# Kernel optimization log

Measured on AMD Instinct MI355X. Metric: run time of the kernel, lower is better.

## Reference

```python
import jax, jax.numpy as jnp
import numpy as np
import math

D_MODEL = 1024
N_HEADS = 16
D_K = 64
D_V = 64
B = 4
S = 1024


def setup_inputs() -> dict:
    key = jax.random.key(0)
    ks = jax.random.split(key, 11)
    # xavier-ish init scale for projections
    s_in = 1.0 / math.sqrt(D_MODEL)
    return {
        "queries": jax.random.normal(ks[0], (B, S, D_MODEL), jnp.float32),
        "keys": jax.random.normal(ks[1], (B, S, D_MODEL), jnp.float32),
        "values": jax.random.normal(ks[2], (B, S, D_MODEL), jnp.float32),
        "Wq": jax.random.normal(ks[3], (D_MODEL, N_HEADS * D_K), jnp.float32) * s_in,
        "bq": jnp.zeros((N_HEADS * D_K,), jnp.float32),
        "Wk": jax.random.normal(ks[4], (D_MODEL, N_HEADS * D_K), jnp.float32) * s_in,
        "bk": jnp.zeros((N_HEADS * D_K,), jnp.float32),
        "Wv": jax.random.normal(ks[5], (D_MODEL, N_HEADS * D_V), jnp.float32) * s_in,
        "bv": jnp.zeros((N_HEADS * D_V,), jnp.float32),
        "Wo": jax.random.normal(ks[6], (N_HEADS * D_V, D_MODEL), jnp.float32) * (1.0 / math.sqrt(N_HEADS * D_V)),
        "bo": jnp.zeros((D_MODEL,), jnp.float32),
    }


def reference(queries, keys, values, Wq, bq, Wk, bk, Wv, bv, Wo, bo):
    Bq, Sq, _ = queries.shape
    Sk = keys.shape[1]
    scale = 1.0 / math.sqrt(D_K)
    # projections -> [B, S, H, d]
    q = (queries @ Wq + bq).reshape(Bq, Sq, N_HEADS, D_K)
    k = (keys @ Wk + bk).reshape(Bq, Sk, N_HEADS, D_K)
    v = (values @ Wv + bv).reshape(Bq, Sk, N_HEADS, D_V)
    # scaled dot-product attention: scores [B, H, Sq, Sk]
    scores = jnp.einsum("bqhd,bkhd->bhqk", q, k) * scale
    attn = jax.nn.softmax(scores, axis=-1)
    # weighted values -> [B, Sq, H*D_V]
    out = jnp.einsum("bhqk,bkhd->bqhd", attn, v).reshape(Bq, Sq, N_HEADS * D_V)
    return out @ Wo + bo
```

## Files before the change

kernel.cpp:

```cpp
#include <hip/hip_runtime.h>
#include <hip/hip_bf16.h>

typedef __attribute__((ext_vector_type(4))) float f32x4;
typedef __attribute__((ext_vector_type(16))) float f32x16;
typedef __attribute__((ext_vector_type(8))) short bf16x8;
typedef __attribute__((ext_vector_type(4))) unsigned short u16x4;
typedef __attribute__((ext_vector_type(8))) unsigned short u16x8;
typedef __attribute__((ext_vector_type(2))) unsigned int u32x2;

#define MFMA16(a, b, c) __builtin_amdgcn_mfma_f32_16x16x32_bf16((a), (b), (c), 0, 0, 0)
#define MFMA32(a, b, c) __builtin_amdgcn_mfma_f32_32x32x16_bf16((a), (b), (c), 0, 0, 0)

static __device__ __forceinline__ unsigned short f2bf(float f) {
    union { float f; unsigned int u; } v; v.f = f;
    unsigned int r = v.u + 0x7FFFu + ((v.u >> 16) & 1u);
    return (unsigned short)(r >> 16);
}
static __device__ __forceinline__ unsigned int pk2(float x, float y) {
    return (unsigned int)f2bf(x) | ((unsigned int)f2bf(y) << 16);
}

static __device__ __forceinline__ void gload_lds16(const void* g, void* l) {
    __builtin_amdgcn_global_load_lds(
        (const __attribute__((address_space(1))) void*)g,
        (__attribute__((address_space(3))) void*)l, 16, 0, 0);
}

__global__ __launch_bounds__(256) void convert_act(
    const float* __restrict__ q, const float* __restrict__ k,
    const float* __restrict__ v, unsigned short* __restrict__ qc,
    unsigned short* __restrict__ kc, unsigned short* __restrict__ vc) {
    const float* src = blockIdx.y == 0 ? q : (blockIdx.y == 1 ? k : v);
    unsigned short* dst = blockIdx.y == 0 ? qc : (blockIdx.y == 1 ? kc : vc);
    size_t off = ((size_t)blockIdx.x * 256 + threadIdx.x) * 8;
    f32x4 a = *(const f32x4*)&src[off];
    f32x4 b = *(const f32x4*)&src[off + 4];
    u16x8 o;
    o[0] = f2bf(a[0]); o[1] = f2bf(a[1]); o[2] = f2bf(a[2]); o[3] = f2bf(a[3]);
    o[4] = f2bf(b[0]); o[5] = f2bf(b[1]); o[6] = f2bf(b[2]); o[7] = f2bf(b[3]);
    *(u16x8*)&dst[off] = o;
}

__global__ __launch_bounds__(256) void transpose_w(
    const float* __restrict__ Wq, const float* __restrict__ Wk,
    const float* __restrict__ Wv, const float* __restrict__ Wo,
    unsigned short* __restrict__ Wt_all, unsigned short* __restrict__ Wot) {
    __shared__ unsigned short T[64][65];
    const int z = blockIdx.z;
    const float* W = z == 0 ? Wq : (z == 1 ? Wk : (z == 2 ? Wv : Wo));
    unsigned short* Wt = z < 3 ? (Wt_all + (size_t)z * 1024 * 1024) : Wot;
    const int k0 = blockIdx.y * 64, n0 = blockIdx.x * 64;
    const int t = threadIdx.x;
    const int rl = t >> 4, c4 = (t & 15) * 4;
#pragma unroll
    for (int i = 0; i < 4; ++i) {
        f32x4 v = *(const f32x4*)&W[(size_t)(k0 + rl + 16 * i) * 1024 + n0 + c4];
#pragma unroll
        for (int j = 0; j < 4; ++j) T[rl + 16 * i][c4 + j] = f2bf(v[j]);
    }
    __syncthreads();
#pragma unroll
    for (int i = 0; i < 4; ++i) {
        u16x4 o;
#pragma unroll
        for (int j = 0; j < 4; ++j) o[j] = T[c4 + j][rl + 16 * i];
        *(u16x4*)&Wt[(size_t)(n0 + rl + 16 * i) * 1024 + k0 + c4] = o;
    }
}

template <bool OUT_BF16>
__global__ __launch_bounds__(256, 2) void gemm_fast(
    const unsigned short* __restrict__ A0, const unsigned short* __restrict__ A1,
    const unsigned short* __restrict__ A2, const unsigned short* __restrict__ Wt,
    const float* __restrict__ b0, const float* __restrict__ b1,
    const float* __restrict__ b2, void* __restrict__ Outv, int ldo) {
    __shared__ __align__(16) unsigned short As[128 * 32];
    __shared__ __align__(16) unsigned short Bs[128 * 32];

    const int t = threadIdx.x;
    const int w = t >> 6, lane = t & 63;
    const int wr = w >> 1, wc = w & 1;
    const int g = lane >> 4, r15 = lane & 15;
    const int bm = blockIdx.y * 128;
    const int bn = blockIdx.x * 128;
    const int msel = bn >> 10;
    const unsigned short* A = msel == 0 ? A0 : (msel == 1 ? A1 : A2);
    const float* bias = msel == 0 ? b0 : (msel == 1 ? b1 : b2);
    const int l4 = lane >> 2, c8 = (lane & 3) * 8;

    f32x4 acc[4][4];
#pragma unroll
    for (int m = 0; m < 4; ++m)
#pragma unroll
        for (int n = 0; n < 4; ++n) acc[m][n] = (f32x4){0.f, 0.f, 0.f, 0.f};

    for (int kt = 0; kt < 1024; kt += 32) {
        __syncthreads();
        gload_lds16(&A[(size_t)(bm + 16 * w + l4) * 1024 + kt + c8], &As[w * 512]);
        gload_lds16(&A[(size_t)(bm + 16 * (w + 4) + l4) * 1024 + kt + c8], &As[(w + 4) * 512]);
        gload_lds16(&Wt[(size_t)(bn + 16 * w + l4) * 1024 + kt + c8], &Bs[w * 512]);
        gload_lds16(&Wt[(size_t)(bn + 16 * (w + 4) + l4) * 1024 + kt + c8], &Bs[(w + 4) * 512]);
        __syncthreads();
        bf16x8 af[4], bfr[4];
#pragma unroll
        for (int m = 0; m < 4; ++m)
            af[m] = *(const bf16x8*)&As[(wr * 64 + m * 16 + r15) * 32 + g * 8];
#pragma unroll
        for (int n = 0; n < 4; ++n)
            bfr[n] = *(const bf16x8*)&Bs[(wc * 64 + n * 16 + r15) * 32 + g * 8];
#pragma unroll
        for (int m = 0; m < 4; ++m)
#pragma unroll
            for (int n = 0; n < 4; ++n)
                acc[m][n] = MFMA16(af[m], bfr[n], acc[m][n]);
    }

    float* Of = (float*)Outv;
    unsigned short* Ob = (unsigned short*)Outv;
#pragma unroll
    for (int n = 0; n < 4; ++n) {
        int col = bn + wc * 64 + n * 16 + r15;
        float bv = bias[col & 1023];
#pragma unroll
        for (int m = 0; m < 4; ++m) {
#pragma unroll
            for (int r = 0; r < 4; ++r) {
                int row = bm + wr * 64 + m * 16 + g * 4 + r;
                float val = acc[m][n][r] + bv;
                if (OUT_BF16)
                    Ob[(size_t)row * ldo + col] = f2bf(val);
                else
                    Of[(size_t)row * ldo + col] = val;
            }
        }
    }
}

template <bool A_BF16, bool OUT_BF16>
__global__ __launch_bounds__(256, 2) void gemm_kernel(
    const void* __restrict__ Av, const float* __restrict__ W,
    const float* __restrict__ bias, void* __restrict__ Outv) {
    __shared__ __align__(16) unsigned short As[128][40];
    __shared__ __align__(16) unsigned short Bs[128][40];

    const int t = threadIdx.x;
    const int bm = blockIdx.y * 128;
    const int bn = blockIdx.x * 128;
    const int w = t >> 6, lane = t & 63;
    const int wr = w >> 1, wc = w & 1;
    const int g = lane >> 4, r15 = lane & 15;

    f32x4 acc[4][4];
#pragma unroll
    for (int m = 0; m < 4; ++m)
#pragma unroll
        for (int n = 0; n < 4; ++n) acc[m][n] = (f32x4){0.f, 0.f, 0.f, 0.f};

    const float* Af = (const float*)Av;
    const unsigned short* Ab = (const unsigned short*)Av;

    for (int kt = 0; kt < 1024; kt += 32) {
        __syncthreads();
#pragma unroll
        for (int i = 0; i < 4; ++i) {
            int row = (t >> 3) + i * 32;
            int c4 = (t & 7) * 4;
            if (A_BF16) {
                u16x4 v = *(const u16x4*)&Ab[(size_t)(bm + row) * 1024 + kt + c4];
                *(u16x4*)&As[row][c4] = v;
            } else {
                f32x4 v = *(const f32x4*)&Af[(size_t)(bm + row) * 1024 + kt + c4];
                u16x4 o;
                o[0] = f2bf(v[0]); o[1] = f2bf(v[1]);
                o[2] = f2bf(v[2]); o[3] = f2bf(v[3]);
                *(u16x4*)&As[row][c4] = o;
            }
        }
#pragma unroll
        for (int i = 0; i < 4; ++i) {
            int k = (t >> 5) + i * 8;
            int c4 = (t & 31) * 4;
            f32x4 v = *(const f32x4*)&W[(size_t)(kt + k) * 1024 + bn + c4];
#pragma unroll
            for (int j = 0; j < 4; ++j) Bs[c4 + j][k] = f2bf(v[j]);
        }
        __syncthreads();
        bf16x8 af[4], bfr[4];
#pragma unroll
        for (int m = 0; m < 4; ++m)
            af[m] = *(const bf16x8*)&As[wr * 64 + m * 16 + r15][g * 8];
#pragma unroll
        for (int n = 0; n < 4; ++n)
            bfr[n] = *(const bf16x8*)&Bs[wc * 64 + n * 16 + r15][g * 8];
#pragma unroll
        for (int m = 0; m < 4; ++m)
#pragma unroll
            for (int n = 0; n < 4; ++n)
                acc[m][n] = MFMA16(af[m], bfr[n], acc[m][n]);
    }

    float* Of = (float*)Outv;
    unsigned short* Ob = (unsigned short*)Outv;
#pragma unroll
    for (int n = 0; n < 4; ++n) {
        int col = bn + wc * 64 + n * 16 + r15;
        float bv = bias[col];
#pragma unroll
        for (int m = 0; m < 4; ++m) {
#pragma unroll
            for (int r = 0; r < 4; ++r) {
                int row = bm + wr * 64 + m * 16 + g * 4 + r;
                float val = acc[m][n][r] + bv;
                if (OUT_BF16)
                    Ob[(size_t)row * 1024 + col] = f2bf(val);
                else
                    Of[(size_t)row * 1024 + col] = val;
            }
        }
    }
}

__global__ __launch_bounds__(256, 2) void attn32_kernel(
    const unsigned short* __restrict__ Q, const unsigned short* __restrict__ K,
    const unsigned short* __restrict__ V, unsigned short* __restrict__ O, int ld) {
    __shared__ __align__(16) unsigned short Kls[2][64 * 80];
    __shared__ __align__(16) unsigned short Vls[2][64 * 80];

    const int t = threadIdx.x;
    const int w = t >> 6, lane = t & 63;
    const int q5 = lane & 31, hi = lane >> 5;

    const int id = blockIdx.x;
    const int sid = (id & 7) * 64 + (id >> 3);
    const int bh = sid >> 3, qb = sid & 7;
    const int b = bh >> 4, h = bh & 15;
    const int brow = b * 1024;
    const int q0 = qb * 128;

    const float c2 = 0.18033688f;

    const unsigned short* Qrow = Q + (size_t)(brow + q0 + w * 32 + q5) * ld + h * 64;
    bf16x8 qreg[8];
#pragma unroll
    for (int j = 0; j < 8; ++j) qreg[j] = *(const bf16x8*)&Qrow[8 * j];
    bf16x8 qsel[4];
#pragma unroll
    for (int kk = 0; kk < 4; ++kk) qsel[kk] = hi ? qreg[2 * kk + 1] : qreg[2 * kk];

    const int krow = t >> 2, kpart = t & 3;
    const int vkey = t & 63, vdc = t >> 6;
    const unsigned short* Kg = K + h * 64;
    const unsigned short* Vg = V + h * 64;

    u16x8 kr0, kr1, vr0, vr1;
#define STG_LOAD(KT)                                                            \
    {                                                                           \
        size_t kro = (size_t)(brow + (KT) + krow) * ld;                         \
        kr0 = *(const u16x8*)&Kg[kro + kpart * 8];                              \
        kr1 = *(const u16x8*)&Kg[kro + kpart * 8 + 32];                         \
        size_t vro = (size_t)(brow + (KT) + vkey) * ld;                         \
        vr0 = *(const u16x8*)&Vg[vro + vdc * 16];                               \
        vr1 = *(const u16x8*)&Vg[vro + vdc * 16 + 8];                           \
    }
#define STG_WRITE(BUF)                                                          \
    {                                                                           \
        char* kb_ = (char*)Kls[BUF];                                            \
        int tg_ = (krow & 7) << 4;                                              \
        *(u16x8*)(kb_ + krow * 160 + ((kpart * 16) ^ tg_)) = kr0;               \
        *(u16x8*)(kb_ + krow * 160 + (((kpart + 4) * 16) ^ tg_)) = kr1;         \
        char* vb_ = (char*)Vls[BUF];                                            \
        _Pragma("unroll") for (int j_ = 0; j_ < 8; ++j_) {                      \
            int d_ = vdc * 16 + j_;                                             \
            *(unsigned short*)(vb_ + d_ * 160 + ((vkey * 2) ^ ((d_ & 7) << 4))) \
                = vr0[j_];                                                      \
        }                                                                       \
        _Pragma("unroll") for (int j_ = 0; j_ < 8; ++j_) {                      \
            int d_ = vdc * 16 + 8 + j_;                                         \
            *(unsigned short*)(vb_ + d_ * 160 + ((vkey * 2) ^ ((d_ & 7) << 4))) \
                = vr1[j_];                                                      \
        }                                                                       \
    }

    f32x16 acc0 = {}, acc1 = {};
    float mrun = -1e30f, lrun = 0.f;

    STG_LOAD(0);
    STG_WRITE(0);
    __syncthreads();

    int cur = 0;
    for (int tile = 0; tile < 16; ++tile) {
        const bool more = tile < 15;
        if (more) STG_LOAD(tile * 64 + 64);

        char* kb = (char*)Kls[cur];
        f32x16 st0 = {}, st1 = {};
        {
            const int tg0 = (q5 & 7) << 4;
            char* kp0 = kb + q5 * 160;
            char* kp1 = kb + (q5 + 32) * 160;
#pragma unroll
            for (int kk = 0; kk < 4; ++kk) {
                int so = ((2 * kk + hi) * 16) ^ tg0;
                bf16x8 kf0 = *(const bf16x8*)(kp0 + so);
                bf16x8 kf1 = *(const bf16x8*)(kp1 + so);
                st0 = MFMA32(kf0, qsel[kk], st0);
                st1 = MFMA32(kf1, qsel[kk], st1);
            }
        }

        float mloc = st0[0];
#pragma unroll
        for (int r = 1; r < 16; ++r) mloc = fmaxf(mloc, st0[r]);
#pragma unroll
        for (int r = 0; r < 16; ++r) mloc = fmaxf(mloc, st1[r]);
        mloc = fmaxf(mloc, __shfl_xor(mloc, 32));
        float mnew = fmaxf(mrun, mloc);
        float sf = exp2f((mrun - mnew) * c2);
        mrun = mnew;
        float mneg = -mrun * c2;
        float rs = 0.f;
#pragma unroll
        for (int r = 0; r < 16; ++r) {
            st0[r] = exp2f(fmaf(st0[r], c2, mneg));
            rs += st0[r];
        }
#pragma unroll
        for (int r = 0; r < 16; ++r) {
            st1[r] = exp2f(fmaf(st1[r], c2, mneg));
            rs += st1[r];
        }
        rs += __shfl_xor(rs, 32);
        lrun = lrun * sf + rs;
#pragma unroll
        for (int r = 0; r < 16; ++r) { acc0[r] *= sf; acc1[r] *= sf; }

        char* vb = (char*)Vls[cur];
        const int tgv = (q5 & 7) << 4;
        char* vp0 = vb + q5 * 160;
        char* vp1 = vb + (q5 + 32) * 160;
#define PV_HALF(ST, CT)                                                         \
    _Pragma("unroll") for (int ks = 0; ks < 2; ++ks) {                          \
        unsigned int a0 = pk2(ST[8 * ks + 0], ST[8 * ks + 1]);                  \
        unsigned int a1 = pk2(ST[8 * ks + 2], ST[8 * ks + 3]);                  \
        unsigned int a2 = pk2(ST[8 * ks + 4], ST[8 * ks + 5]);                  \
        unsigned int a3 = pk2(ST[8 * ks + 6], ST[8 * ks + 7]);                  \
        unsigned int x0 = __shfl_xor(a0, 32), x1 = __shfl_xor(a1, 32);          \
        unsigned int x2 = __shfl_xor(a2, 32), x3 = __shfl_xor(a3, 32);          \
        union { unsigned int u[4]; bf16x8 v; } pfu;                             \
        pfu.u[0] = hi ? x2 : a0;                                                \
        pfu.u[1] = hi ? x3 : a1;                                                \
        pfu.u[2] = hi ? a2 : x0;                                                \
        pfu.u[3] = hi ? a3 : x1;                                                \
        int co = ((32 * (2 * (CT) + ks) + 16 * hi)) ^ tgv;                      \
        bf16x8 vf0 = *(const bf16x8*)(vp0 + co);                                \
        bf16x8 vf1 = *(const bf16x8*)(vp1 + co);                                \
        acc0 = MFMA32(vf0, pfu.v, acc0);                                        \
        acc1 = MFMA32(vf1, pfu.v, acc1);                                        \
    }
        PV_HALF(st0, 0);
        PV_HALF(st1, 1);

        if (more) STG_WRITE(cur ^ 1);
        __syncthreads();
        cur ^= 1;
    }

    const float inv = 1.0f / lrun;
    unsigned short* Orow = O + (size_t)(brow + q0 + w * 32 + q5) * 1024 + h * 64;
#pragma unroll
    for (int k = 0; k < 4; ++k) {
        int d0 = 8 * k + 4 * hi;
        u32x2 pa, pb;
        pa[0] = pk2(acc0[4 * k + 0] * inv, acc0[4 * k + 1] * inv);
        pa[1] = pk2(acc0[4 * k + 2] * inv, acc0[4 * k + 3] * inv);
        *(u32x2*)&Orow[d0] = pa;
        pb[0] = pk2(acc1[4 * k + 0] * inv, acc1[4 * k + 1] * inv);
        pb[1] = pk2(acc1[4 * k + 2] * inv, acc1[4 * k + 3] * inv);
        *(u32x2*)&Orow[32 + d0] = pb;
    }
#undef STG_LOAD
#undef STG_WRITE
#undef PV_HALF
}

extern "C" void kernel_launch(void* const* d_in, const int* in_sizes, int n_in,
                              void* d_out, int out_size, void* d_ws, size_t ws_size,
                              hipStream_t stream) {
    const float* q  = (const float*)d_in[0];
    const float* k  = (const float*)d_in[1];
    const float* v  = (const float*)d_in[2];
    const float* Wq = (const float*)d_in[3];
    const float* bq = (const float*)d_in[4];
    const float* Wk = (const float*)d_in[5];
    const float* bk = (const float*)d_in[6];
    const float* Wv = (const float*)d_in[7];
    const float* bv = (const float*)d_in[8];
    const float* Wo = (const float*)d_in[9];
    const float* bo = (const float*)d_in[10];

    const size_t M1 = (size_t)1024 * 1024;
    const size_t NEED = 28 * M1 * sizeof(unsigned short);

    dim3 bt(256, 1, 1);
    if (ws_size >= NEED) {
        unsigned short* qc  = (unsigned short*)d_ws;
        unsigned short* kc  = qc + 4 * M1;
        unsigned short* vc  = kc + 4 * M1;
        unsigned short* Wt  = vc + 4 * M1;
        unsigned short* Wot = Wt + 3 * M1;
        unsigned short* QKV = Wot + M1;
        unsigned short* Ob  = qc;

        convert_act<<<dim3(2048, 3), bt, 0, stream>>>(q, k, v, qc, kc, vc);
        transpose_w<<<dim3(16, 16, 4), bt, 0, stream>>>(Wq, Wk, Wv, Wo, Wt, Wot);
        gemm_fast<true><<<dim3(24, 32), bt, 0, stream>>>(qc, kc, vc, Wt, bq, bk, bv, QKV, 3072);
        attn32_kernel<<<dim3(512), bt, 0, stream>>>(QKV, QKV + 1024, QKV + 2048, Ob, 3072);
        gemm_fast<false><<<dim3(8, 32), bt, 0, stream>>>(Ob, Ob, Ob, Wot, bo, bo, bo, d_out, 1024);
    } else {
        const size_t NE = (size_t)4096 * 1024;
        unsigned short* Qb = (unsigned short*)d_ws;
        unsigned short* Kb = Qb + NE;
        unsigned short* Vb = Kb + NE;
        unsigned short* Ob = Vb + NE;
        dim3 gg(8, 32);
        gemm_kernel<false, true><<<gg, bt, 0, stream>>>(q, Wq, bq, Qb);
        gemm_kernel<false, true><<<gg, bt, 0, stream>>>(k, Wk, bk, Kb);
        gemm_kernel<false, true><<<gg, bt, 0, stream>>>(v, Wv, bv, Vb);
        attn32_kernel<<<dim3(512), bt, 0, stream>>>(Qb, Kb, Vb, Ob, 1024);
        gemm_kernel<true, false><<<gg, bt, 0, stream>>>(Ob, Wo, bo, d_out);
    }
}
```

Baseline: 229.6 us.

## Use hardware bf16 pack, lazy softmax rescale, setprio, paired V staging, narrower output GEMM tile

Replaces the software bf16 rounding with the v_cvt_pk_bf16_f32 instruction in the conversion and attention paths. In attention, the V staging now loads two adjacent keys per thread and writes packed 32-bit LDS stores. The online-softmax rescale is skipped unless the running max rises by more than a threshold, and MFMA sections are wrapped in s_setprio. The output projection GEMM uses a 64-wide N tile, giving 512 blocks instead of 256 for better CU coverage at the cost of less B-operand reuse per block.

```diff
diff --git a/kernel.cpp b/kernel.cpp
--- a/kernel.cpp
+++ b/kernel.cpp
@@ -17,7 +17,9 @@
     return (unsigned short)(r >> 16);
 }
 static __device__ __forceinline__ unsigned int pk2(float x, float y) {
-    return (unsigned int)f2bf(x) | ((unsigned int)f2bf(y) << 16);
+    unsigned int r;
+    asm("v_cvt_pk_bf16_f32 %0, %1, %2" : "=v"(r) : "v"(x), "v"(y));
+    return r;
 }
 
 static __device__ __forceinline__ void gload_lds16(const void* g, void* l) {
@@ -35,10 +37,10 @@
     size_t off = ((size_t)blockIdx.x * 256 + threadIdx.x) * 8;
     f32x4 a = *(const f32x4*)&src[off];
     f32x4 b = *(const f32x4*)&src[off + 4];
-    u16x8 o;
-    o[0] = f2bf(a[0]); o[1] = f2bf(a[1]); o[2] = f2bf(a[2]); o[3] = f2bf(a[3]);
-    o[4] = f2bf(b[0]); o[5] = f2bf(b[1]); o[6] = f2bf(b[2]); o[7] = f2bf(b[3]);
-    *(u16x8*)&dst[off] = o;
+    union { unsigned int u[4]; u16x8 v; } o;
+    o.u[0] = pk2(a[0], a[1]); o.u[1] = pk2(a[2], a[3]);
+    o.u[2] = pk2(b[0], b[1]); o.u[3] = pk2(b[2], b[3]);
+    *(u16x8*)&dst[off] = o.v;
 }
 
 __global__ __launch_bounds__(256) void transpose_w(
@@ -68,58 +70,64 @@
     }
 }
 
-template <bool OUT_BF16>
+template <bool OUT_BF16, int BN>
 __global__ __launch_bounds__(256, 2) void gemm_fast(
     const unsigned short* __restrict__ A0, const unsigned short* __restrict__ A1,
     const unsigned short* __restrict__ A2, const unsigned short* __restrict__ Wt,
     const float* __restrict__ b0, const float* __restrict__ b1,
     const float* __restrict__ b2, void* __restrict__ Outv, int ldo) {
+    constexpr int NF = BN / 32;
     __shared__ __align__(16) unsigned short As[128 * 32];
-    __shared__ __align__(16) unsigned short Bs[128 * 32];
+    __shared__ __align__(16) unsigned short Bs[BN * 32];
 
     const int t = threadIdx.x;
     const int w = t >> 6, lane = t & 63;
     const int wr = w >> 1, wc = w & 1;
     const int g = lane >> 4, r15 = lane & 15;
     const int bm = blockIdx.y * 128;
-    const int bn = blockIdx.x * 128;
+    const int bn = blockIdx.x * BN;
     const int msel = bn >> 10;
     const unsigned short* A = msel == 0 ? A0 : (msel == 1 ? A1 : A2);
     const float* bias = msel == 0 ? b0 : (msel == 1 ? b1 : b2);
     const int l4 = lane >> 2, c8 = (lane & 3) * 8;
 
-    f32x4 acc[4][4];
+    f32x4 acc[4][NF];
 #pragma unroll
     for (int m = 0; m < 4; ++m)
 #pragma unroll
-        for (int n = 0; n < 4; ++n) acc[m][n] = (f32x4){0.f, 0.f, 0.f, 0.f};
+        for (int n = 0; n < NF; ++n) acc[m][n] = (f32x4){0.f, 0.f, 0.f, 0.f};
 
     for (int kt = 0; kt < 1024; kt += 32) {
         __syncthreads();
         gload_lds16(&A[(size_t)(bm + 16 * w + l4) * 1024 + kt + c8], &As[w * 512]);
         gload_lds16(&A[(size_t)(bm + 16 * (w + 4) + l4) * 1024 + kt + c8], &As[(w + 4) * 512]);
-        gload_lds16(&Wt[(size_t)(bn + 16 * w + l4) * 1024 + kt + c8], &Bs[w * 512]);
-        gload_lds16(&Wt[(size_t)(bn + 16 * (w + 4) + l4) * 1024 + kt + c8], &Bs[(w + 4) * 512]);
+        if (BN == 128) {
+            gload_lds16(&Wt[(size_t)(bn + 16 * w + l4) * 1024 + kt + c8], &Bs[w * 512]);
+            gload_lds16(&Wt[(size_t)(bn + 16 * (w + 4) + l4) * 1024 + kt + c8],
+                        &Bs[(w + 4) * 512 % (BN * 32)]);
+        } else {
+            gload_lds16(&Wt[(size_t)(bn + 16 * w + l4) * 1024 + kt + c8], &Bs[w * 512]);
+        }
         __syncthreads();
-        bf16x8 af[4], bfr[4];
+        bf16x8 af[4], bfr[NF];
 #pragma unroll
         for (int m = 0; m < 4; ++m)
             af[m] = *(const bf16x8*)&As[(wr * 64 + m * 16 + r15) * 32 + g * 8];
 #pragma unroll
-        for (int n = 0; n < 4; ++n)
-            bfr[n] = *(const bf16x8*)&Bs[(wc * 64 + n * 16 + r15) * 32 + g * 8];
+        for (int n = 0; n < NF; ++n)
+            bfr[n] = *(const bf16x8*)&Bs[(wc * (BN / 2) + n * 16 + r15) * 32 + g * 8];
 #pragma unroll
         for (int m = 0; m < 4; ++m)
 #pragma unroll
-            for (int n = 0; n < 4; ++n)
+            for (int n = 0; n < NF; ++n)
                 acc[m][n] = MFMA16(af[m], bfr[n], acc[m][n]);
     }
 
     float* Of = (float*)Outv;
     unsigned short* Ob = (unsigned short*)Outv;
 #pragma unroll
-    for (int n = 0; n < 4; ++n) {
-        int col = bn + wc * 64 + n * 16 + r15;
+    for (int n = 0; n < NF; ++n) {
+        int col = bn + wc * (BN / 2) + n * 16 + r15;
         float bv = bias[col & 1023];
 #pragma unroll
         for (int m = 0; m < 4; ++m) {
@@ -248,7 +256,7 @@
     for (int kk = 0; kk < 4; ++kk) qsel[kk] = hi ? qreg[2 * kk + 1] : qreg[2 * kk];
 
     const int krow = t >> 2, kpart = t & 3;
-    const int vkey = t & 63, vdc = t >> 6;
+    const int vp = t & 31, vdc = t >> 5;
     const unsigned short* Kg = K + h * 64;
     const unsigned short* Vg = V + h * 64;
 
@@ -258,9 +266,9 @@
         size_t kro = (size_t)(brow + (KT) + krow) * ld;                         \
         kr0 = *(const u16x8*)&Kg[kro + kpart * 8];                              \
         kr1 = *(const u16x8*)&Kg[kro + kpart * 8 + 32];                         \
-        size_t vro = (size_t)(brow + (KT) + vkey) * ld;                         \
-        vr0 = *(const u16x8*)&Vg[vro + vdc * 16];                               \
-        vr1 = *(const u16x8*)&Vg[vro + vdc * 16 + 8];                           \
+        size_t vro = (size_t)(brow + (KT) + 2 * vp) * ld;                       \
+        vr0 = *(const u16x8*)&Vg[vro + vdc * 8];                                \
+        vr1 = *(const u16x8*)&Vg[vro + ld + vdc * 8];                           \
     }
 #define STG_WRITE(BUF)                                                          \
     {                                                                           \
@@ -270,14 +278,11 @@
         *(u16x8*)(kb_ + krow * 160 + (((kpart + 4) * 16) ^ tg_)) = kr1;         \
         char* vb_ = (char*)Vls[BUF];                                            \
         _Pragma("unroll") for (int j_ = 0; j_ < 8; ++j_) {                      \
-            int d_ = vdc * 16 + j_;                                             \
-            *(unsigned short*)(vb_ + d_ * 160 + ((vkey * 2) ^ ((d_ & 7) << 4))) \
-                = vr0[j_];                                                      \
-        }                                                                       \
-        _Pragma("unroll") for (int j_ = 0; j_ < 8; ++j_) {                      \
-            int d_ = vdc * 16 + 8 + j_;                                         \
-            *(unsigned short*)(vb_ + d_ * 160 + ((vkey * 2) ^ ((d_ & 7) << 4))) \
-                = vr1[j_];                                                      \
+            int d_ = vdc * 8 + j_;                                              \
+            unsigned int pk_ = (unsigned int)(unsigned short)vr0[j_] |          \
+                               ((unsigned int)(unsigned short)vr1[j_] << 16);   \
+            *(unsigned int*)(vb_ + d_ * 160 + ((vp * 4) ^ ((d_ & 7) << 4)))     \
+                = pk_;                                                          \
         }                                                                       \
     }
 
@@ -299,6 +304,7 @@
             const int tg0 = (q5 & 7) << 4;
             char* kp0 = kb + q5 * 160;
             char* kp1 = kb + (q5 + 32) * 160;
+            __builtin_amdgcn_s_setprio(1);
 #pragma unroll
             for (int kk = 0; kk < 4; ++kk) {
                 int so = ((2 * kk + hi) * 16) ^ tg0;
@@ -307,17 +313,23 @@
                 st0 = MFMA32(kf0, qsel[kk], st0);
                 st1 = MFMA32(kf1, qsel[kk], st1);
             }
-        }
-
-        float mloc = st0[0];
-#pragma unroll
-        for (int r = 1; r < 16; ++r) mloc = fmaxf(mloc, st0[r]);
+            __builtin_amdgcn_s_setprio(0);
+        }
+
+        float mloc = fmaxf(st0[0], st0[1]);
+#pragma unroll
+        for (int r = 2; r < 16; ++r) mloc = fmaxf(mloc, st0[r]);
 #pragma unroll
         for (int r = 0; r < 16; ++r) mloc = fmaxf(mloc, st1[r]);
         mloc = fmaxf(mloc, __shfl_xor(mloc, 32));
-        float mnew = fmaxf(mrun, mloc);
-        float sf = exp2f((mrun - mnew) * c2);
-        mrun = mnew;
+        if (!__all(mloc - mrun <= 64.f)) {
+            float mnew = fmaxf(mrun, mloc);
+            float sf = exp2f((mrun - mnew) * c2);
+            mrun = mnew;
+            lrun *= sf;
+#pragma unroll
+            for (int r = 0; r < 16; ++r) { acc0[r] *= sf; acc1[r] *= sf; }
+        }
         float mneg = -mrun * c2;
         float rs = 0.f;
 #pragma unroll
@@ -331,14 +343,13 @@
             rs += st1[r];
         }
         rs += __shfl_xor(rs, 32);
-        lrun = lrun * sf + rs;
-#pragma unroll
-        for (int r = 0; r < 16; ++r) { acc0[r] *= sf; acc1[r] *= sf; }
+        lrun += rs;
 
         char* vb = (char*)Vls[cur];
         const int tgv = (q5 & 7) << 4;
         char* vp0 = vb + q5 * 160;
         char* vp1 = vb + (q5 + 32) * 160;
+        __builtin_amdgcn_s_setprio(1);
 #define PV_HALF(ST, CT)                                                         \
     _Pragma("unroll") for (int ks = 0; ks < 2; ++ks) {                          \
         unsigned int a0 = pk2(ST[8 * ks + 0], ST[8 * ks + 1]);                  \
@@ -360,6 +371,7 @@
     }
         PV_HALF(st0, 0);
         PV_HALF(st1, 1);
+        __builtin_amdgcn_s_setprio(0);
 
         if (more) STG_WRITE(cur ^ 1);
         __syncthreads();
@@ -414,9 +426,9 @@
 
         convert_act<<<dim3(2048, 3), bt, 0, stream>>>(q, k, v, qc, kc, vc);
         transpose_w<<<dim3(16, 16, 4), bt, 0, stream>>>(Wq, Wk, Wv, Wo, Wt, Wot);
-        gemm_fast<true><<<dim3(24, 32), bt, 0, stream>>>(qc, kc, vc, Wt, bq, bk, bv, QKV, 3072);
+        gemm_fast<true, 128><<<dim3(24, 32), bt, 0, stream>>>(qc, kc, vc, Wt, bq, bk, bv, QKV, 3072);
         attn32_kernel<<<dim3(512), bt, 0, stream>>>(QKV, QKV + 1024, QKV + 2048, Ob, 3072);
-        gemm_fast<false><<<dim3(8, 32), bt, 0, stream>>>(Ob, Ob, Ob, Wot, bo, bo, bo, d_out, 1024);
+        gemm_fast<false, 64><<<dim3(16, 32), bt, 0, stream>>>(Ob, Ob, Ob, Wot, bo, bo, bo, d_out, 1024);
     } else {
         const size_t NE = (size_t)4096 * 1024;
         unsigned short* Qb = (unsigned short*)d_ws;
```

After: 217.6 us. 1.06x faster.
